# Kernel optimization log

Hardware: AMD Instinct MI355X
Metric: run time of the kernel (lower is better)

Reference implementation:

```python
import jax, jax.numpy as jnp
import numpy as np

N = 100000   # nodes
E = 3200000  # directed edges
F = 16       # num_features (colors)


def setup_inputs() -> dict:
    key = jax.random.key(0)
    ks = jax.random.split(key, 5)
    x = jax.random.normal(ks[0], (N, F), dtype=jnp.float32)
    edge_index = jax.random.randint(ks[1], (2, E), 0, N)
    # Glorot-ish scaled weights for the 5 identical blocks (F->64->32->F)
    W1 = jax.random.normal(ks[2], (5, F, 64), dtype=jnp.float32) * (1.0 / np.sqrt(F))
    W2 = jax.random.normal(ks[3], (5, 64, 32), dtype=jnp.float32) * (1.0 / np.sqrt(64))
    W3 = jax.random.normal(ks[4], (5, 32, F), dtype=jnp.float32) * (1.0 / np.sqrt(32))
    b1 = jnp.zeros((5, 64), dtype=jnp.float32)
    b2 = jnp.zeros((5, 32), dtype=jnp.float32)
    b3 = jnp.zeros((5, F), dtype=jnp.float32)
    return {"x": x, "edge_index": edge_index,
            "W1": W1, "b1": b1, "W2": W2, "b2": b2, "W3": W3, "b3": b3}


def _gcn(x, W, b, src, dst, norm, n):
    # GCNConv: project, then symmetric-normalized neighbor sum (self-loops in src/dst)
    h = x @ W                                   # [n, d_out]
    msg = h[src] * norm[:, None]                # [e+n, d_out] gather + scale
    out = jax.ops.segment_sum(msg, dst, num_segments=n)
    return out + b


def reference(x, edge_index, W1, b1, W2, b2, W3, b3):
    n = x.shape[0]
    loops = jnp.arange(n)
    src = jnp.concatenate([edge_index[0], loops])  # add self loops (PyG default)
    dst = jnp.concatenate([edge_index[1], loops])
    deg = jax.ops.segment_sum(jnp.ones(src.shape[0], jnp.float32), dst, num_segments=n)
    dis = jax.lax.rsqrt(jnp.maximum(deg, 1.0))     # deg >= 1 due to self loops
    norm = dis[src] * dis[dst]
    for i in range(5):
        x = jax.nn.relu(_gcn(x, W1[i], b1[i], src, dst, norm, n))
        x = jax.nn.relu(_gcn(x, W2[i], b2[i], src, dst, norm, n))
        x = jax.nn.softmax(_gcn(x, W3[i], b3[i], src, dst, norm, n), axis=1)
    return x
```

## Files before the change

### kernel.cpp

```cpp
#include <hip/hip_runtime.h>

#define NN 100000
#define NE 3200000
#define SLAB 80
#define SLAB4 (SLAB / 4)
#define NB 196
#define BSH 9
#define BCAP 20480
#define NBB 1024
#define EPB 3125

typedef int      vi4 __attribute__((ext_vector_type(4)));
typedef float    vf4 __attribute__((ext_vector_type(4)));
typedef _Float16 vh8 __attribute__((ext_vector_type(8)));


__global__ __launch_bounds__(256)
void k_bucket(const int* __restrict__ src, const int* __restrict__ dst,
              int* __restrict__ gcur, int* __restrict__ entries) {
    __shared__ int scnt[NB];
    __shared__ int sofs[NB];
    __shared__ int sbase[NB];
    __shared__ int sfill[NB];
    __shared__ int tmp[256];
    __shared__ int stage[EPB];
    int tid = threadIdx.x;
    for (int i = tid; i < NB; i += 256) { scnt[i] = 0; sfill[i] = 0; }
    __syncthreads();
    int e0 = blockIdx.x * EPB;
    int e1 = e0 + EPB;
    for (int e = e0 + tid; e < e1; e += 256)
        atomicAdd(&scnt[__builtin_nontemporal_load(dst + e) >> BSH], 1);
    __syncthreads();
    tmp[tid] = (tid < NB) ? scnt[tid] : 0;
    __syncthreads();
    #pragma unroll
    for (int o = 1; o < 256; o <<= 1) {
        int v = (tid >= o) ? tmp[tid - o] : 0;
        __syncthreads();
        tmp[tid] += v;
        __syncthreads();
    }
    if (tid < NB) {
        sofs[tid] = tmp[tid] - scnt[tid];
        sbase[tid] = atomicAdd(&gcur[tid], scnt[tid]);
    }
    __syncthreads();
    for (int e = e0 + tid; e < e1; e += 256) {
        int d = __builtin_nontemporal_load(dst + e);
        int s = __builtin_nontemporal_load(src + e);
        int b = d >> BSH;
        int pos = sofs[b] + atomicAdd(&sfill[b], 1);
        stage[pos] = s | ((d & 511) << 17);
    }
    __syncthreads();
    int wid = tid >> 6, lane = tid & 63;
    for (int b = wid; b < NB; b += 4) {
        int cnt = scnt[b];
        int gbase = sbase[b];
        int lbase = sofs[b];
        for (int j = lane; j < cnt; j += 64) {
            int pos = gbase + j;
            if (pos < BCAP)
                __builtin_nontemporal_store(stage[lbase + j], entries + b * BCAP + pos);
        }
    }
}

__global__ __launch_bounds__(512)
void k_csr(const int* __restrict__ gcur, const int* __restrict__ entries,
           int* __restrict__ col, int* __restrict__ cnt4, float* __restrict__ dis,
           const float* __restrict__ x, vh8* __restrict__ xs8,
           vh8* __restrict__ h3s8, vh8* __restrict__ h2s8) {
    __shared__ int lcur[512];
    int tid = threadIdx.x;
    int b = blockIdx.x;
    lcur[tid] = 0;
    __syncthreads();
    int nE = min(gcur[b], BCAP);
    const int* ep = entries + b * BCAP;
    int nbase = b << BSH;
    for (int e = tid; e < nE; e += 512) {
        int v = __builtin_nontemporal_load(ep + e);
        int s = v & 0x1FFFF;
        int local = v >> 17;
        int p = atomicAdd(&lcur[local], 1);
        if (p < SLAB) col[(size_t)(nbase + local) * SLAB + p] = s;
    }
    __syncthreads();
    {
        int node = nbase + tid;
        if (node < NN) {
            int c = lcur[tid];
            float dn = rsqrtf((float)(c + 1));
            dis[node] = dn;
            int cc = min(c, SLAB);
            int c4 = (cc + 3) >> 2;
            cnt4[node] = c4;
            int* slab = col + (size_t)node * SLAB;
            for (int k = cc; k < c4 * 4; k++) slab[k] = NN;
            const vf4* xr = (const vf4*)(x + (size_t)node * 16);
            vh8 o0, o1;
            #pragma unroll
            for (int i = 0; i < 4; i++) {
                o0[i]     = (_Float16)(xr[0][i] * dn);
                o0[i + 4] = (_Float16)(xr[1][i] * dn);
                o1[i]     = (_Float16)(xr[2][i] * dn);
                o1[i + 4] = (_Float16)(xr[3][i] * dn);
            }
            xs8[(size_t)node * 2 + 0] = o0;
            xs8[(size_t)node * 2 + 1] = o1;
        }
    }
    if (b == 0 && tid < 8) {
        vh8 z = {(_Float16)0.f, (_Float16)0.f, (_Float16)0.f, (_Float16)0.f,
                 (_Float16)0.f, (_Float16)0.f, (_Float16)0.f, (_Float16)0.f};
        if (tid < 2)      xs8[NN * 2 + tid] = z;
        else if (tid < 4) h3s8[NN * 2 + (tid - 2)] = z;
        else              h2s8[NN * 4 + (tid - 4)] = z;
    }
}

template<int CH, int UNROLL>
__device__ inline void gather4w(const vh8* __restrict__ in, const int4* __restrict__ cp,
                                int c4, int node, int d, int h, float* acc) {
    vh8 self = in[node * CH + d];
    #pragma unroll
    for (int i = 0; i < 8; i++) acc[i] = h ? 0.f : (float)self[i];
    #pragma unroll UNROLL
    for (int k = h; k < c4; k += 4) {
        vi4 cs = __builtin_nontemporal_load((const vi4*)(cp + k));
        vh8 a = in[cs.x * CH + d];
        vh8 b = in[cs.y * CH + d];
        vh8 c = in[cs.z * CH + d];
        vh8 e = in[cs.w * CH + d];
        #pragma unroll
        for (int i = 0; i < 8; i++)
            acc[i] += ((float)a[i] + (float)b[i]) + ((float)c[i] + (float)e[i]);
    }
    #pragma unroll
    for (int i = 0; i < 8; i++) acc[i] += __shfl_xor(acc[i], 1);
    #pragma unroll
    for (int i = 0; i < 8; i++) acc[i] += __shfl_xor(acc[i], 2);
}


__global__ __launch_bounds__(256)
void k_layerA(const vh8* __restrict__ xs, const int* __restrict__ cnt4,
              const int4* __restrict__ colv, const float* __restrict__ dis,
              const float* __restrict__ W1, const float* __restrict__ b1,
              const float* __restrict__ W2, _Float16* __restrict__ h2s) {
    __shared__ float sW1[16 * 64];
    __shared__ float sW2[64 * 32];
    __shared__ float sb1[64];
    __shared__ float st[32 * 16];
    __shared__ _Float16 sx1h[32 * 72];
    int tid = threadIdx.x;
    for (int i = tid; i < 16 * 64; i += 256) sW1[i] = W1[i];
    for (int i = tid; i < 64 * 32; i += 256) sW2[i] = W2[i];
    if (tid < 64) sb1[tid] = b1[tid];

    int nl = tid >> 3, ll = tid & 7, d = ll >> 2, h = ll & 3;
    int node = blockIdx.x * 32 + nl;
    float dn = dis[node];
    float acc[8];
    gather4w<2, 2>(xs, colv + (size_t)node * SLAB4, cnt4[node], node, d, h, acc);
    if (h == 0) {
        vf4 v0 = {acc[0] * dn, acc[1] * dn, acc[2] * dn, acc[3] * dn};
        vf4 v1 = {acc[4] * dn, acc[5] * dn, acc[6] * dn, acc[7] * dn};
        ((vf4*)st)[nl * 4 + d * 2 + 0] = v0;
        ((vf4*)st)[nl * 4 + d * 2 + 1] = v1;
    }
    __syncthreads();

    int c = tid & 63, g = tid >> 6;
    #pragma unroll
    for (int p = 0; p < 2; p++) {
        int nb = g * 8 + p * 4;
        float a0 = sb1[c], a1 = a0, a2 = a0, a3 = a0;
        #pragma unroll
        for (int k = 0; k < 16; k++) {
            float w = sW1[k * 64 + c];
            a0 += st[(nb + 0) * 16 + k] * w;
            a1 += st[(nb + 1) * 16 + k] * w;
            a2 += st[(nb + 2) * 16 + k] * w;
            a3 += st[(nb + 3) * 16 + k] * w;
        }
        sx1h[(nb + 0) * 72 + c] = (_Float16)fmaxf(a0, 0.f);
        sx1h[(nb + 1) * 72 + c] = (_Float16)fmaxf(a1, 0.f);
        sx1h[(nb + 2) * 72 + c] = (_Float16)fmaxf(a2, 0.f);
        sx1h[(nb + 3) * 72 + c] = (_Float16)fmaxf(a3, 0.f);
    }
    __syncthreads();

    int c2 = tid & 31, g2 = tid >> 5;
    #pragma unroll
    for (int p = 0; p < 4; p++) {
        int n2 = g2 * 4 + p;
        const vh8* xr = (const vh8*)(sx1h + n2 * 72);
        float a = 0.f;
        #pragma unroll
        for (int j = 0; j < 8; j++) {
            vh8 v = xr[j];
            #pragma unroll
            for (int i = 0; i < 8; i++)
                a += (float)v[i] * sW2[(j * 8 + i) * 32 + c2];
        }
        int gn = blockIdx.x * 32 + n2;
        h2s[(size_t)gn * 32 + c2] = (_Float16)(a * dis[gn]);
    }
}

__global__ __launch_bounds__(256)
void k_aggmm3(const vh8* __restrict__ h2s, const int* __restrict__ cnt4,
              const int4* __restrict__ colv, const float* __restrict__ dis,
              const float* __restrict__ b2, const float* __restrict__ W3,
              _Float16* __restrict__ h3s) {
    __shared__ float sW[32 * 16];
    __shared__ float sb[32];
    __shared__ float st[16 * 40];
    int tid = threadIdx.x;
    for (int i = tid; i < 32 * 16; i += 256) sW[i] = W3[i];
    if (tid < 32) sb[tid] = b2[tid];
    __syncthreads();

    int nl = tid >> 4, ll = tid & 15, d = ll >> 2, h = ll & 3;
    int node = blockIdx.x * 16 + nl;
    float dn = dis[node];
    float acc[8];
    gather4w<4, 2>(h2s, colv + (size_t)node * SLAB4, cnt4[node], node, d, h, acc);
    if (h == 0) {
        vf4 v0, v1;
        #pragma unroll
        for (int i = 0; i < 4; i++) {
            v0[i] = fmaxf(acc[i] * dn + sb[d * 8 + i], 0.f);
            v1[i] = fmaxf(acc[i + 4] * dn + sb[d * 8 + 4 + i], 0.f);
        }
        vf4* sp = (vf4*)(st + nl * 40 + d * 8);
        sp[0] = v0;
        sp[1] = v1;
    }
    __syncthreads();

    int c = tid & 15, n = tid >> 4;
    float a0 = 0.f;
    #pragma unroll
    for (int k = 0; k < 32; k++) a0 += st[n * 40 + k] * sW[k * 16 + c];
    int gn = blockIdx.x * 16 + n;
    h3s[(size_t)gn * 16 + c] = (_Float16)(a0 * dis[gn]);
}

__global__ __launch_bounds__(256)
void k_agg_soft(const vh8* __restrict__ in, const int* __restrict__ cnt4,
                const int4* __restrict__ colv, const float* __restrict__ dis,
                const float* __restrict__ bias, float* __restrict__ out,
                vh8* __restrict__ out2) {
    int tid = threadIdx.x;
    int nl = tid >> 3, ll = tid & 7, d = ll >> 2, h = ll & 3;
    int node = blockIdx.x * 32 + nl;
    float dn = dis[node];
    float acc[8];
    gather4w<2, 2>(in, colv + (size_t)node * SLAB4, cnt4[node], node, d, h, acc);
    #pragma unroll
    for (int i = 0; i < 8; i++) acc[i] = acc[i] * dn + bias[d * 8 + i];
    float m = acc[0];
    #pragma unroll
    for (int i = 1; i < 8; i++) m = fmaxf(m, acc[i]);
    m = fmaxf(m, __shfl_xor(m, 4));
    float ev[8], s = 0.f;
    #pragma unroll
    for (int i = 0; i < 8; i++) { ev[i] = __expf(acc[i] - m); s += ev[i]; }
    s += __shfl_xor(s, 4);
    float inv = 1.0f / s;
    if (h == 0) {
        vf4 o0 = {ev[0] * inv, ev[1] * inv, ev[2] * inv, ev[3] * inv};
        vf4 o1 = {ev[4] * inv, ev[5] * inv, ev[6] * inv, ev[7] * inv};
        __builtin_nontemporal_store(o0, (vf4*)out + (size_t)node * 4 + d * 2);
        __builtin_nontemporal_store(o1, (vf4*)out + (size_t)node * 4 + d * 2 + 1);
        vh8 ho;
        #pragma unroll
        for (int i = 0; i < 8; i++) ho[i] = (_Float16)(ev[i] * inv * dn);
        out2[(size_t)node * 2 + d] = ho;
    }
}


static inline size_t align_up(size_t v, size_t a) { return (v + a - 1) & ~(a - 1); }

extern "C" void kernel_launch(void* const* d_in, const int* in_sizes, int n_in,
                              void* d_out, int out_size, void* d_ws, size_t ws_size,
                              hipStream_t stream) {
    const float* x   = (const float*)d_in[0];
    const int*   ei  = (const int*)d_in[1];
    const float* W1  = (const float*)d_in[2];
    const float* b1  = (const float*)d_in[3];
    const float* W2  = (const float*)d_in[4];
    const float* b2  = (const float*)d_in[5];
    const float* W3  = (const float*)d_in[6];
    const float* b3  = (const float*)d_in[7];
    float* outp = (float*)d_out;

    const int* src = ei;
    const int* dst = ei + NE;

    char* ws = (char*)d_ws;
    size_t off = 0;
    auto carve = [&](size_t bytes) { void* p = ws + off; off = align_up(off + bytes, 256); return p; };
    int*      gcur  = (int*)     carve(NB * 4);
    int*      cnt4  = (int*)     carve(NN * 4);
    float*    dis   = (float*)   carve(NN * 4);
    int*      col   = (int*)     carve((size_t)NN * SLAB * 4);
    _Float16* xs    = (_Float16*)carve((size_t)(NN + 1) * 16 * 2);
    _Float16* h3s   = (_Float16*)carve((size_t)(NN + 1) * 16 * 2);
    int*      entries = (int*)   carve((size_t)NB * BCAP * 4);
    _Float16* h2s   = (_Float16*)carve((size_t)(NN + 1) * 32 * 2);
    (void)ws_size; (void)n_in; (void)in_sizes; (void)out_size;

    hipMemsetAsync(gcur, 0, NB * 4, stream);
    k_bucket<<<NBB, 256, 0, stream>>>(src, dst, gcur, entries);
    k_csr<<<NB, 512, 0, stream>>>(gcur, entries, col, cnt4, dis, x,
                                  (vh8*)xs, (vh8*)h3s, (vh8*)h2s);

    const int gA = NN / 32;
    const int gB = NN / 16;
    const int gC = NN / 32;

    for (int l = 0; l < 5; l++) {
        k_layerA<<<gA, 256, 0, stream>>>((const vh8*)xs, cnt4, (const int4*)col, dis,
                                         W1 + l * 16 * 64, b1 + l * 64, W2 + l * 64 * 32, h2s);
        k_aggmm3<<<gB, 256, 0, stream>>>((const vh8*)h2s, cnt4, (const int4*)col, dis,
                                         b2 + l * 32, W3 + l * 32 * 16, h3s);
        k_agg_soft<<<gC, 256, 0, stream>>>((const vh8*)h3s, cnt4, (const int4*)col, dis,
                                           b3 + l * 16, outp, (vh8*)xs);
    }
}
```

Measured before the change: 705.9 us.

## Single-pass edge bucketing with fixed-capacity LDS slots and global overflow

Replaces the two-pass count/prefix-scan/scatter bucketing with a single pass. Each edge gets a slot in a fixed 64-entry per-bucket LDS area, and overflow edges are written straight to global memory through a global atomic. The edge arrays are read once with vectorized int4 loads, using 500 blocks of 512 threads that each take 6400 edges. Each block's average of about 33 edges per bucket fits in the slots, so overflow should be rare. The cost is possible global-atomic traffic and uncoalesced writes when the slots fill up.

```diff
diff --git a/kernel.cpp b/kernel.cpp
--- a/kernel.cpp
+++ b/kernel.cpp
@@ -7,62 +7,61 @@
 #define NB 196
 #define BSH 9
 #define BCAP 20480
-#define NBB 1024
-#define EPB 3125
+#define NBB 500
+#define EPB 6400
+#define CAP 64
 
 typedef int      vi4 __attribute__((ext_vector_type(4)));
 typedef float    vf4 __attribute__((ext_vector_type(4)));
 typedef _Float16 vh8 __attribute__((ext_vector_type(8)));
 
 
-__global__ __launch_bounds__(256)
+__global__ __launch_bounds__(512)
 void k_bucket(const int* __restrict__ src, const int* __restrict__ dst,
               int* __restrict__ gcur, int* __restrict__ entries) {
-    __shared__ int scnt[NB];
-    __shared__ int sofs[NB];
+    __shared__ int stage[NB * CAP];
+    __shared__ int sfill[NB];
     __shared__ int sbase[NB];
-    __shared__ int sfill[NB];
-    __shared__ int tmp[256];
-    __shared__ int stage[EPB];
-    int tid = threadIdx.x;
-    for (int i = tid; i < NB; i += 256) { scnt[i] = 0; sfill[i] = 0; }
-    __syncthreads();
+    int tid = threadIdx.x;
+    for (int i = tid; i < NB; i += 512) sfill[i] = 0;
+    __syncthreads();
+
     int e0 = blockIdx.x * EPB;
-    int e1 = e0 + EPB;
-    for (int e = e0 + tid; e < e1; e += 256)
-        atomicAdd(&scnt[__builtin_nontemporal_load(dst + e) >> BSH], 1);
-    __syncthreads();
-    tmp[tid] = (tid < NB) ? scnt[tid] : 0;
-    __syncthreads();
-    #pragma unroll
-    for (int o = 1; o < 256; o <<= 1) {
-        int v = (tid >= o) ? tmp[tid - o] : 0;
-        __syncthreads();
-        tmp[tid] += v;
-        __syncthreads();
-    }
+    const vi4* d4 = (const vi4*)(dst + e0);
+    const vi4* s4 = (const vi4*)(src + e0);
+    for (int i = tid; i < EPB / 4; i += 512) {
+        vi4 dv = __builtin_nontemporal_load(d4 + i);
+        vi4 sv = __builtin_nontemporal_load(s4 + i);
+        #pragma unroll
+        for (int j = 0; j < 4; j++) {
+            int d = dv[j];
+            int b = d >> BSH;
+            int v = sv[j] | ((d & 511) << 17);
+            int p = atomicAdd(&sfill[b], 1);
+            if (p < CAP) {
+                stage[b * CAP + p] = v;
+            } else {
+                int gp = atomicAdd(&gcur[b], 1);
+                if (gp < BCAP) entries[b * BCAP + gp] = v;
+            }
+        }
+    }
+    __syncthreads();
+
     if (tid < NB) {
-        sofs[tid] = tmp[tid] - scnt[tid];
-        sbase[tid] = atomicAdd(&gcur[tid], scnt[tid]);
-    }
-    __syncthreads();
-    for (int e = e0 + tid; e < e1; e += 256) {
-        int d = __builtin_nontemporal_load(dst + e);
-        int s = __builtin_nontemporal_load(src + e);
-        int b = d >> BSH;
-        int pos = sofs[b] + atomicAdd(&sfill[b], 1);
-        stage[pos] = s | ((d & 511) << 17);
-    }
-    __syncthreads();
+        int cnt = min(sfill[tid], CAP);
+        sbase[tid] = atomicAdd(&gcur[tid], cnt);
+    }
+    __syncthreads();
+
     int wid = tid >> 6, lane = tid & 63;
-    for (int b = wid; b < NB; b += 4) {
-        int cnt = scnt[b];
+    for (int b = wid; b < NB; b += 8) {
+        int cnt = min(sfill[b], CAP);
         int gbase = sbase[b];
-        int lbase = sofs[b];
         for (int j = lane; j < cnt; j += 64) {
             int pos = gbase + j;
             if (pos < BCAP)
-                __builtin_nontemporal_store(stage[lbase + j], entries + b * BCAP + pos);
+                __builtin_nontemporal_store(stage[b * CAP + j], entries + b * BCAP + pos);
         }
     }
 }
@@ -317,7 +316,7 @@
     (void)ws_size; (void)n_in; (void)in_sizes; (void)out_size;
 
     hipMemsetAsync(gcur, 0, NB * 4, stream);
-    k_bucket<<<NBB, 256, 0, stream>>>(src, dst, gcur, entries);
+    k_bucket<<<NBB, 512, 0, stream>>>(src, dst, gcur, entries);
     k_csr<<<NB, 512, 0, stream>>>(gcur, entries, col, cnt4, dis, x,
                                   (vh8*)xs, (vh8*)h3s, (vh8*)h2s);
 
```

Result: faster. 678.2 us (-3.9%).
